# Kernel tuning notes

Hardware: AMD Instinct MI355X
Metric: run time of the kernel (lower is better)

Reference implementation:

```python
import jax, jax.numpy as jnp
import numpy as np

B, S, D = 4, 2048, 1024

def setup_inputs() -> dict:
    key = jax.random.key(0)
    ks = jax.random.split(key, 9)
    sc = 1.0 / np.sqrt(D)
    return {
        "x": jax.random.normal(ks[0], (B, S, D), dtype=jnp.float32),
        "Wq": jax.random.normal(ks[1], (D, D), dtype=jnp.float32) * sc,
        "bq": jnp.zeros((D,), dtype=jnp.float32),
        "Wk": jax.random.normal(ks[2], (D, D), dtype=jnp.float32) * sc,
        "bk": jnp.zeros((D,), dtype=jnp.float32),
        "Wv": jax.random.normal(ks[3], (D, D), dtype=jnp.float32) * sc,
        "bv": jnp.zeros((D,), dtype=jnp.float32),
        "Wo": jax.random.normal(ks[4], (D, D), dtype=jnp.float32) * sc,
        "bo": jnp.zeros((D,), dtype=jnp.float32),
    }

def _gaussian_mask(seq_len, dtype):
    # exp(-0.5*((pos - S/2)/(S/4))^2), shape [1,1,S] -> broadcasts over KEY axis
    pos = jnp.arange(seq_len, dtype=dtype)
    center = seq_len / 2
    sigma = seq_len / 4
    m = jnp.exp(-0.5 * ((pos - center) / sigma) ** 2)
    return m[None, None, :]

def reference(x, Wq, bq, Wk, bk, Wv, bv, Wo, bo):
    d = x.shape[-1]
    Q = x @ Wq.T + bq            # [B,S,D]
    K = x @ Wk.T + bk
    V = x @ Wv.T + bv
    scores = jnp.einsum('bqd,bkd->bqk', Q, K) / jnp.sqrt(jnp.asarray(d, x.dtype))
    scores = scores * _gaussian_mask(x.shape[1], x.dtype)
    attn = jax.nn.softmax(scores, axis=-1)
    out = jnp.einsum('bqk,bkd->bqd', attn, V)
    return out @ Wo.T + bo
```

## Files before the change

### kernel.cpp

```cpp
#include <hip/hip_runtime.h>
#include <math.h>

#define SEQ 2048
#define DIM 1024

typedef __attribute__((ext_vector_type(8))) _Float16 half8;
typedef __attribute__((ext_vector_type(4))) float f32x4;

__device__ __forceinline__ unsigned short f2h(float f) {
    union { _Float16 h; unsigned short u; } c; c.h = (_Float16)f;
    return c.u;
}
__device__ __forceinline__ float gmask(int k) {
    float t = ((float)k - 1024.0f) * (1.0f / 512.0f);
    return expf(-0.5f * t * t);
}
__device__ __forceinline__ void glds16(const unsigned short* gp, unsigned short* lp) {
    __builtin_amdgcn_global_load_lds((const __attribute__((address_space(1))) void*)gp,
                                     (__attribute__((address_space(3))) void*)lp, 16, 0, 0);
}

__device__ __forceinline__ void stage64(const unsigned short* __restrict__ g, int ldK,
                                        unsigned short* lds, int wave, int lane) {
    int row = wave * 32 + (lane >> 3);
    int seg = (lane & 7) ^ (lane >> 3);
    const unsigned short* gp = g + (long)row * ldK + seg * 8;
    unsigned short* lp = lds + wave * 2048;
    glds16(gp, lp);
    glds16(gp + 8 * (long)ldK, lp + 512);
    glds16(gp + 16 * (long)ldK, lp + 1024);
    glds16(gp + 24 * (long)ldK, lp + 1536);
}

enum { EPI_QKV = 0, EPI_EXP = 1, EPI_PV = 2, EPI_OUT = 3 };

template <int EPI>
__global__ __launch_bounds__(256, 4) void mfma_gemm(
    const unsigned short* __restrict__ A, const unsigned short* __restrict__ Bm,
    const float* __restrict__ bias,
    float* __restrict__ Cf, unsigned short* __restrict__ Ch,
    int M, int N, int K, float scale, long sA, long sB, long sC)
{
    __shared__ unsigned short As[128 * 64];
    __shared__ unsigned short Bs[128 * 64];

    const int bz = blockIdx.z;
    const int tid = threadIdx.x;
    const int wave = tid >> 6;
    const int lane = tid & 63;
    const int wm = (wave & 1) * 64;
    const int wn = (wave >> 1) * 64;
    const long m0 = (long)blockIdx.y * 128;
    const long n0 = (long)blockIdx.x * 128;
    const int lm = lane & 15;
    const int lk = lane >> 4;

    const unsigned short* pA = A + bz * sA + m0 * K;
    const unsigned short* pB = Bm + bz * sB + n0 * K;

    f32x4 acc[4][4];
#pragma unroll
    for (int i = 0; i < 4; ++i)
#pragma unroll
        for (int j = 0; j < 4; ++j) {
            acc[i][j].x = 0.f; acc[i][j].y = 0.f; acc[i][j].z = 0.f; acc[i][j].w = 0.f;
        }

    int aoff[4][2], boff[4][2];
#pragma unroll
    for (int i = 0; i < 4; ++i)
#pragma unroll
        for (int t = 0; t < 2; ++t) {
            int ar = wm + i * 16 + lm;
            aoff[i][t] = ar * 64 + (((4 * t + lk) ^ (ar & 7)) << 3);
            int br = wn + i * 16 + lm;
            boff[i][t] = br * 64 + (((4 * t + lk) ^ (br & 7)) << 3);
        }

    const int pr = (wave & 1) * 64 + lane;
    const int ph = wave >> 1;
    float psum = 0.f;

    for (int k0 = 0; k0 < K; k0 += 64) {
        stage64(pA + k0, K, As, wave, lane);
        stage64(pB + k0, K, Bs, wave, lane);
        __syncthreads();

        if (EPI == EPI_PV) {
            const unsigned short* rowp = As + pr * 64;
#pragma unroll
            for (int i2 = 0; i2 < 4; ++i2) {
                half8 h = *(const half8*)(rowp + (((2 * i2 + ph) ^ (pr & 7)) << 3));
#pragma unroll
                for (int e = 0; e < 8; ++e) psum += (float)h[e];
            }
        }

#pragma unroll
        for (int t = 0; t < 2; ++t) {
            half8 a[4], b[4];
#pragma unroll
            for (int i = 0; i < 4; ++i) a[i] = *(const half8*)(As + aoff[i][t]);
#pragma unroll
            for (int j = 0; j < 4; ++j) b[j] = *(const half8*)(Bs + boff[j][t]);
#pragma unroll
            for (int i = 0; i < 4; ++i)
#pragma unroll
                for (int j = 0; j < 4; ++j)
                    acc[i][j] = __builtin_amdgcn_mfma_f32_16x16x32_f16(a[i], b[j], acc[i][j], 0, 0, 0);
        }
        __syncthreads();
    }

    float* rsf = (float*)As;
    if (EPI == EPI_PV) {
        rsf[ph * 128 + pr] = psum;
        __syncthreads();
    }

    const long MD = 8388608;
    float* cF = (EPI == EPI_OUT) ? Cf + bz * sC : (float*)nullptr;
    unsigned short* cH = (EPI != EPI_OUT) ? Ch + bz * sC : (unsigned short*)nullptr;

#pragma unroll
    for (int i = 0; i < 4; ++i) {
        long mrow = m0 + wm + i * 16 + lk * 4;
        int lr = wm + i * 16 + lk * 4;
        float inv4[4];
        if (EPI == EPI_PV) {
#pragma unroll
            for (int r = 0; r < 4; ++r)
                inv4[r] = 1.0f / (rsf[lr + r] + rsf[128 + lr + r]);
        }
#pragma unroll
        for (int j = 0; j < 4; ++j) {
            int n = (int)n0 + wn + j * 16 + lm;
            if (EPI == EPI_QKV) {
                int sel = n >> 10;
                int n1 = n & 1023;
                float bs = bias[n];
                if (sel < 2) {
                    unsigned short* dst = cH + (long)sel * MD;
#pragma unroll
                    for (int r = 0; r < 4; ++r)
                        dst[(mrow + r) * (long)DIM + n1] = f2h(acc[i][j][r] + bs);
                } else {
                    long b = mrow >> 11, s = mrow & 2047;
                    long idx = 2 * MD + b * (long)DIM * SEQ + (long)n1 * SEQ + s;
                    unsigned long long pk =
                        (unsigned long long)f2h(acc[i][j].x + bs) |
                        ((unsigned long long)f2h(acc[i][j].y + bs) << 16) |
                        ((unsigned long long)f2h(acc[i][j].z + bs) << 32) |
                        ((unsigned long long)f2h(acc[i][j].w + bs) << 48);
                    *(unsigned long long*)(cH + idx) = pk;
                }
            } else if (EPI == EPI_EXP) {
                float mult = scale * gmask(n);
#pragma unroll
                for (int r = 0; r < 4; ++r)
                    cH[(mrow + r) * (long)N + n] = f2h(expf(acc[i][j][r] * mult));
            } else if (EPI == EPI_PV) {
#pragma unroll
                for (int r = 0; r < 4; ++r)
                    cH[(mrow + r) * (long)N + n] = f2h(acc[i][j][r] * inv4[r]);
            } else {
                float bs = bias[n];
#pragma unroll
                for (int r = 0; r < 4; ++r)
                    cF[(mrow + r) * (long)N + n] = acc[i][j][r] + bs;
            }
        }
    }
}

__global__ __launch_bounds__(256) void prep(
    const float* __restrict__ x,
    const float* __restrict__ Wq, const float* __restrict__ Wk,
    const float* __restrict__ Wv, const float* __restrict__ Wo,
    const float* __restrict__ b0, const float* __restrict__ b1, const float* __restrict__ b2,
    unsigned short* __restrict__ xh, unsigned short* __restrict__ Wp, float* __restrict__ bqkv)
{
    long gid = (long)blockIdx.x * 256 + threadIdx.x;
    if (gid < 3072) {
        int sel = (int)(gid >> 10);
        const float* s = sel == 0 ? b0 : sel == 1 ? b1 : b2;
        bqkv[gid] = s[gid & 1023];
    }
    const long NX = 8388608 / 4;
    const long NW = 1048576 / 4;
    const long total = NX + 4 * NW;
    for (long i = gid; i < total; i += (long)gridDim.x * 256) {
        const float* src; unsigned short* dst; long off;
        if (i < NX) { src = x; dst = xh; off = i; }
        else {
            long wi = i - NX;
            int sel = (int)(wi >> 18);
            src = sel == 0 ? Wq : sel == 1 ? Wk : sel == 2 ? Wv : Wo;
            dst = Wp + ((long)sel << 20);
            off = wi & (NW - 1);
        }
        float4 v = ((const float4*)src)[off];
        unsigned long long p = (unsigned long long)f2h(v.x) | ((unsigned long long)f2h(v.y) << 16) |
                               ((unsigned long long)f2h(v.z) << 32) | ((unsigned long long)f2h(v.w) << 48);
        ((unsigned long long*)dst)[off] = p;
    }
}

extern "C" void kernel_launch(void* const* d_in, const int* in_sizes, int n_in,
                              void* d_out, int out_size, void* d_ws, size_t ws_size,
                              hipStream_t stream)
{
    const float* x  = (const float*)d_in[0];
    const float* Wq = (const float*)d_in[1];
    const float* bq = (const float*)d_in[2];
    const float* Wk = (const float*)d_in[3];
    const float* bk = (const float*)d_in[4];
    const float* Wv = (const float*)d_in[5];
    const float* bv = (const float*)d_in[6];
    const float* Wo = (const float*)d_in[7];
    const float* bo = (const float*)d_in[8];
    float* out = (float*)d_out;

    const long MD = 4L * SEQ * DIM;
    const long WW = (long)DIM * DIM;
    const long SD = (long)SEQ * DIM, SS = (long)SEQ * SEQ;

    unsigned short* xh   = (unsigned short*)d_ws;
    unsigned short* Wp   = xh + MD;
    unsigned short* Woh  = Wp + 3 * WW;
    float* bqkv          = (float*)(Wp + 4 * WW);
    unsigned short* Qh   = (unsigned short*)(bqkv + 4096);
    unsigned short* VT   = Qh + 2 * MD;
    unsigned short* expS = Qh + 3 * MD;
    unsigned short* O1   = xh;

    dim3 blk(256);
    prep<<<4096, blk, 0, stream>>>(x, Wq, Wk, Wv, Wo, bq, bk, bv, xh, Wp, bqkv);

    mfma_gemm<EPI_QKV><<<dim3(3 * DIM / 128, (4 * SEQ) / 128, 1), blk, 0, stream>>>(
        xh, Wp, bqkv, nullptr, Qh, 4 * SEQ, 3 * DIM, DIM, 1.0f, 0, 0, 0);
    mfma_gemm<EPI_EXP><<<dim3(SEQ / 128, SEQ / 128, 4), blk, 0, stream>>>(
        Qh, Qh + MD, nullptr, nullptr, expS, SEQ, SEQ, DIM, 0.03125f, SD, SD, SS);
    mfma_gemm<EPI_PV><<<dim3(DIM / 128, SEQ / 128, 4), blk, 0, stream>>>(
        expS, VT, nullptr, nullptr, O1, SEQ, DIM, SEQ, 1.0f, SS, (long)DIM * SEQ, SD);
    mfma_gemm<EPI_OUT><<<dim3(DIM / 128, (4 * SEQ) / 128, 1), blk, 0, stream>>>(
        O1, Woh, bo, out, nullptr, 4 * SEQ, DIM, DIM, 1.0f, 0, 0, 0);
}
```

Before: 270.6 us.

## Pipeline GEMM with triple-buffered LDS, 128x256 tiles, and row sums moved to exp epilogue

Rewrites the shared MFMA GEMM to use 512-thread blocks computing 128x256 tiles. A three-stage LDS ring buffer with async global-to-LDS loads interleaves staging with MFMA phases, using explicit barriers, waitcnt and setprio to overlap memory and compute. The softmax row-sum is now computed in the exp epilogue via shuffles and atomics into a zeroed buffer, replacing the per-tile LDS reduction in the PV kernel. This adds more barriers per iteration and atomic traffic, and raises LDS usage, which may limit occupancy.

```diff
diff --git a/kernel.cpp b/kernel.cpp
--- a/kernel.cpp
+++ b/kernel.cpp
@@ -11,6 +11,10 @@
     union { _Float16 h; unsigned short u; } c; c.h = (_Float16)f;
     return c.u;
 }
+__device__ __forceinline__ float h2f(unsigned short u) {
+    union { unsigned short u2; _Float16 h; } c; c.u2 = u;
+    return (float)c.h;
+}
 __device__ __forceinline__ float gmask(int k) {
     float t = ((float)k - 1024.0f) * (1.0f / 512.0f);
     return expf(-0.5f * t * t);
@@ -20,38 +24,40 @@
                                      (__attribute__((address_space(3))) void*)lp, 16, 0, 0);
 }
 
-__device__ __forceinline__ void stage64(const unsigned short* __restrict__ g, int ldK,
-                                        unsigned short* lds, int wave, int lane) {
-    int row = wave * 32 + (lane >> 3);
+__device__ __forceinline__ void stage_unit(const unsigned short* __restrict__ g, int ldK,
+                                           unsigned short* lds, int wave, int lane) {
+    int row = wave * 16 + (lane >> 3);
     int seg = (lane & 7) ^ (lane >> 3);
     const unsigned short* gp = g + (long)row * ldK + seg * 8;
-    unsigned short* lp = lds + wave * 2048;
+    unsigned short* lp = lds + wave * 1024;
     glds16(gp, lp);
     glds16(gp + 8 * (long)ldK, lp + 512);
-    glds16(gp + 16 * (long)ldK, lp + 1024);
-    glds16(gp + 24 * (long)ldK, lp + 1536);
 }
 
 enum { EPI_QKV = 0, EPI_EXP = 1, EPI_PV = 2, EPI_OUT = 3 };
 
+#define BAR() __builtin_amdgcn_s_barrier()
+#define LGKM0() asm volatile("s_waitcnt lgkmcnt(0)" ::: "memory")
+#define VMC(N) asm volatile("s_waitcnt vmcnt(" #N ")" ::: "memory")
+
 template <int EPI>
-__global__ __launch_bounds__(256, 4) void mfma_gemm(
+__global__ __launch_bounds__(512, 2) void mfma_gemm(
     const unsigned short* __restrict__ A, const unsigned short* __restrict__ Bm,
-    const float* __restrict__ bias,
+    const float* __restrict__ aux,
     float* __restrict__ Cf, unsigned short* __restrict__ Ch,
+    float* __restrict__ rsum,
     int M, int N, int K, float scale, long sA, long sB, long sC)
 {
-    __shared__ unsigned short As[128 * 64];
-    __shared__ unsigned short Bs[128 * 64];
+    __shared__ unsigned short sh[3 * 24576];
 
     const int bz = blockIdx.z;
     const int tid = threadIdx.x;
     const int wave = tid >> 6;
     const int lane = tid & 63;
-    const int wm = (wave & 1) * 64;
-    const int wn = (wave >> 1) * 64;
+    const int rb = (wave & 1) * 64;
+    const int cb = (wave >> 1) * 64;
     const long m0 = (long)blockIdx.y * 128;
-    const long n0 = (long)blockIdx.x * 128;
+    const long n0 = (long)blockIdx.x * 256;
     const int lm = lane & 15;
     const int lk = lane >> 4;
 
@@ -68,54 +74,103 @@
 
     int aoff[4][2], boff[4][2];
 #pragma unroll
-    for (int i = 0; i < 4; ++i)
+    for (int f = 0; f < 4; ++f)
 #pragma unroll
         for (int t = 0; t < 2; ++t) {
-            int ar = wm + i * 16 + lm;
-            aoff[i][t] = ar * 64 + (((4 * t + lk) ^ (ar & 7)) << 3);
-            int br = wn + i * 16 + lm;
-            boff[i][t] = br * 64 + (((4 * t + lk) ^ (br & 7)) << 3);
-        }
-
-    const int pr = (wave & 1) * 64 + lane;
-    const int ph = wave >> 1;
-    float psum = 0.f;
-
-    for (int k0 = 0; k0 < K; k0 += 64) {
-        stage64(pA + k0, K, As, wave, lane);
-        stage64(pB + k0, K, Bs, wave, lane);
-        __syncthreads();
-
-        if (EPI == EPI_PV) {
-            const unsigned short* rowp = As + pr * 64;
-#pragma unroll
-            for (int i2 = 0; i2 < 4; ++i2) {
-                half8 h = *(const half8*)(rowp + (((2 * i2 + ph) ^ (pr & 7)) << 3));
-#pragma unroll
-                for (int e = 0; e < 8; ++e) psum += (float)h[e];
-            }
-        }
-
-#pragma unroll
-        for (int t = 0; t < 2; ++t) {
-            half8 a[4], b[4];
-#pragma unroll
-            for (int i = 0; i < 4; ++i) a[i] = *(const half8*)(As + aoff[i][t]);
-#pragma unroll
-            for (int j = 0; j < 4; ++j) b[j] = *(const half8*)(Bs + boff[j][t]);
-#pragma unroll
-            for (int i = 0; i < 4; ++i)
-#pragma unroll
-                for (int j = 0; j < 4; ++j)
-                    acc[i][j] = __builtin_amdgcn_mfma_f32_16x16x32_f16(a[i], b[j], acc[i][j], 0, 0, 0);
-        }
-        __syncthreads();
-    }
-
-    float* rsf = (float*)As;
-    if (EPI == EPI_PV) {
-        rsf[ph * 128 + pr] = psum;
-        __syncthreads();
+            int ar = rb + f * 16 + lm;
+            aoff[f][t] = ar * 64 + (((4 * t + lk) ^ (ar & 7)) << 3);
+            int br = cb + f * 16 + lm;
+            boff[f][t] = br * 64 + (((4 * t + lk) ^ (br & 7)) << 3);
+        }
+
+    const int NT = K >> 6;
+
+    stage_unit(pA, K, sh, wave, lane);
+    stage_unit(pB, K, sh + 8192, wave, lane);
+    stage_unit(pB + 128 * (long)K, K, sh + 16384, wave, lane);
+    stage_unit(pA + 64, K, sh + 24576, wave, lane);
+    stage_unit(pB + 64, K, sh + 24576 + 8192, wave, lane);
+    stage_unit(pB + 128 * (long)K + 64, K, sh + 24576 + 16384, wave, lane);
+    VMC(6);
+    BAR();
+
+#pragma unroll 1
+    for (int t = 0; t < NT; ++t) {
+        unsigned short* As = sh + (t % 3) * 24576;
+        unsigned short* Bs = As + 8192;
+        const int t2 = t + 2;
+        const bool st = t2 < NT;
+        unsigned short* Sd = sh + (t2 % 3) * 24576;
+
+        half8 a[2][2], b[4][2];
+
+#pragma unroll
+        for (int kt = 0; kt < 2; ++kt) {
+            a[0][kt] = *(const half8*)(As + aoff[0][kt]);
+            a[1][kt] = *(const half8*)(As + aoff[1][kt]);
+            b[0][kt] = *(const half8*)(Bs + boff[0][kt]);
+            b[1][kt] = *(const half8*)(Bs + boff[1][kt]);
+        }
+        if (st) stage_unit(pA + t2 * 64, K, Sd, wave, lane);
+        BAR(); LGKM0();
+        __builtin_amdgcn_s_setprio(1);
+#pragma unroll
+        for (int mi = 0; mi < 2; ++mi)
+#pragma unroll
+            for (int nj = 0; nj < 2; ++nj)
+#pragma unroll
+                for (int kt = 0; kt < 2; ++kt)
+                    acc[mi][nj] = __builtin_amdgcn_mfma_f32_16x16x32_f16(a[mi][kt], b[nj][kt], acc[mi][nj], 0, 0, 0);
+        __builtin_amdgcn_s_setprio(0);
+        BAR();
+
+#pragma unroll
+        for (int kt = 0; kt < 2; ++kt) {
+            b[2][kt] = *(const half8*)(Bs + boff[2][kt]);
+            b[3][kt] = *(const half8*)(Bs + boff[3][kt]);
+        }
+        if (st) stage_unit(pB + t2 * 64, K, Sd + 8192, wave, lane);
+        BAR(); LGKM0();
+        __builtin_amdgcn_s_setprio(1);
+#pragma unroll
+        for (int mi = 0; mi < 2; ++mi)
+#pragma unroll
+            for (int nj = 2; nj < 4; ++nj)
+#pragma unroll
+                for (int kt = 0; kt < 2; ++kt)
+                    acc[mi][nj] = __builtin_amdgcn_mfma_f32_16x16x32_f16(a[mi][kt], b[nj][kt], acc[mi][nj], 0, 0, 0);
+        __builtin_amdgcn_s_setprio(0);
+        BAR();
+
+#pragma unroll
+        for (int kt = 0; kt < 2; ++kt) {
+            a[0][kt] = *(const half8*)(As + aoff[2][kt]);
+            a[1][kt] = *(const half8*)(As + aoff[3][kt]);
+        }
+        if (st) stage_unit(pB + 128 * (long)K + t2 * 64, K, Sd + 16384, wave, lane);
+        BAR(); LGKM0();
+        __builtin_amdgcn_s_setprio(1);
+#pragma unroll
+        for (int mi = 0; mi < 2; ++mi)
+#pragma unroll
+            for (int nj = 2; nj < 4; ++nj)
+#pragma unroll
+                for (int kt = 0; kt < 2; ++kt)
+                    acc[2 + mi][nj] = __builtin_amdgcn_mfma_f32_16x16x32_f16(a[mi][kt], b[nj][kt], acc[2 + mi][nj], 0, 0, 0);
+        __builtin_amdgcn_s_setprio(0);
+        BAR();
+
+        __builtin_amdgcn_s_setprio(1);
+#pragma unroll
+        for (int mi = 0; mi < 2; ++mi)
+#pragma unroll
+            for (int nj = 0; nj < 2; ++nj)
+#pragma unroll
+                for (int kt = 0; kt < 2; ++kt)
+                    acc[2 + mi][nj] = __builtin_amdgcn_mfma_f32_16x16x32_f16(a[mi][kt], b[nj][kt], acc[2 + mi][nj], 0, 0, 0);
+        __builtin_amdgcn_s_setprio(0);
+        if (t < NT - 2) { VMC(6); } else { VMC(0); }
+        BAR();
     }
 
     const long MD = 8388608;
@@ -123,51 +178,74 @@
     unsigned short* cH = (EPI != EPI_OUT) ? Ch + bz * sC : (unsigned short*)nullptr;
 
 #pragma unroll
-    for (int i = 0; i < 4; ++i) {
-        long mrow = m0 + wm + i * 16 + lk * 4;
-        int lr = wm + i * 16 + lk * 4;
-        float inv4[4];
-        if (EPI == EPI_PV) {
-#pragma unroll
-            for (int r = 0; r < 4; ++r)
-                inv4[r] = 1.0f / (rsf[lr + r] + rsf[128 + lr + r]);
-        }
-#pragma unroll
-        for (int j = 0; j < 4; ++j) {
-            int n = (int)n0 + wn + j * 16 + lm;
-            if (EPI == EPI_QKV) {
+    for (int mf = 0; mf < 4; ++mf) {
+        long mrow = m0 + rb + mf * 16 + lk * 4;
+        if (EPI == EPI_QKV) {
+#pragma unroll
+            for (int nf = 0; nf < 4; ++nf) {
+                int n = (int)n0 + cb + nf * 16 + lm;
                 int sel = n >> 10;
                 int n1 = n & 1023;
-                float bs = bias[n];
+                float bs = aux[n];
                 if (sel < 2) {
                     unsigned short* dst = cH + (long)sel * MD;
 #pragma unroll
                     for (int r = 0; r < 4; ++r)
-                        dst[(mrow + r) * (long)DIM + n1] = f2h(acc[i][j][r] + bs);
+                        dst[(mrow + r) * (long)DIM + n1] = f2h(acc[mf][nf][r] + bs);
                 } else {
-                    long b = mrow >> 11, s = mrow & 2047;
-                    long idx = 2 * MD + b * (long)DIM * SEQ + (long)n1 * SEQ + s;
+                    long bb = mrow >> 11, s = mrow & 2047;
+                    long idx = 2 * MD + bb * (long)DIM * SEQ + (long)n1 * SEQ + s;
                     unsigned long long pk =
-                        (unsigned long long)f2h(acc[i][j].x + bs) |
-                        ((unsigned long long)f2h(acc[i][j].y + bs) << 16) |
-                        ((unsigned long long)f2h(acc[i][j].z + bs) << 32) |
-                        ((unsigned long long)f2h(acc[i][j].w + bs) << 48);
+                        (unsigned long long)f2h(acc[mf][nf].x + bs) |
+                        ((unsigned long long)f2h(acc[mf][nf].y + bs) << 16) |
+                        ((unsigned long long)f2h(acc[mf][nf].z + bs) << 32) |
+                        ((unsigned long long)f2h(acc[mf][nf].w + bs) << 48);
                     *(unsigned long long*)(cH + idx) = pk;
                 }
-            } else if (EPI == EPI_EXP) {
+            }
+        } else if (EPI == EPI_EXP) {
+            float rsv[4] = {0.f, 0.f, 0.f, 0.f};
+#pragma unroll
+            for (int nf = 0; nf < 4; ++nf) {
+                int n = (int)n0 + cb + nf * 16 + lm;
                 float mult = scale * gmask(n);
 #pragma unroll
+                for (int r = 0; r < 4; ++r) {
+                    float e = expf(acc[mf][nf][r] * mult);
+                    unsigned short h = f2h(e);
+                    cH[(mrow + r) * (long)N + n] = h;
+                    rsv[r] += h2f(h);
+                }
+            }
+#pragma unroll
+            for (int r = 0; r < 4; ++r) {
+#pragma unroll
+                for (int msk = 1; msk < 16; msk <<= 1)
+                    rsv[r] += __shfl_xor(rsv[r], msk, 64);
+            }
+            if (lm == 0) {
+#pragma unroll
                 for (int r = 0; r < 4; ++r)
-                    cH[(mrow + r) * (long)N + n] = f2h(expf(acc[i][j][r] * mult));
-            } else if (EPI == EPI_PV) {
+                    atomicAdd(rsum + (long)bz * SEQ + mrow + r, rsv[r]);
+            }
+        } else if (EPI == EPI_PV) {
+#pragma unroll
+            for (int r = 0; r < 4; ++r) {
+                float inv = 1.0f / rsum[(long)bz * SEQ + mrow + r];
+#pragma unroll
+                for (int nf = 0; nf < 4; ++nf) {
+                    int n = (int)n0 + cb + nf * 16 + lm;
+                    cH[(mrow + r) * (long)N + n] = f2h(acc[mf][nf][r] * inv);
+                }
+            }
+        } else {
+#pragma unroll
+            for (int nf = 0; nf < 4; ++nf) {
+                int n = (int)n0 + cb + nf * 16 + lm;
+                float bs = aux[n];
 #pragma unroll
                 for (int r = 0; r < 4; ++r)
-                    cH[(mrow + r) * (long)N + n] = f2h(acc[i][j][r] * inv4[r]);
-            } else {
-                float bs = bias[n];
-#pragma unroll
-                for (int r = 0; r < 4; ++r)
-                    cF[(mrow + r) * (long)N + n] = acc[i][j][r] + bs;
+                    cF[(mrow + r) * (long)N + n] = acc[mf][nf][r] + bs;
             }
         }
     }
@@ -178,7 +256,8 @@
     const float* __restrict__ Wq, const float* __restrict__ Wk,
     const float* __restrict__ Wv, const float* __restrict__ Wo,
     const float* __restrict__ b0, const float* __restrict__ b1, const float* __restrict__ b2,
-    unsigned short* __restrict__ xh, unsigned short* __restrict__ Wp, float* __restrict__ bqkv)
+    unsigned short* __restrict__ xh, unsigned short* __restrict__ Wp,
+    float* __restrict__ bqkv, float* __restrict__ rsum)
 {
     long gid = (long)blockIdx.x * 256 + threadIdx.x;
     if (gid < 3072) {
@@ -186,6 +265,7 @@
         const float* s = sel == 0 ? b0 : sel == 1 ? b1 : b2;
         bqkv[gid] = s[gid & 1023];
     }
+    if (gid < 4 * SEQ) rsum[gid] = 0.f;
     const long NX = 8388608 / 4;
     const long NW = 1048576 / 4;
     const long total = NX + 4 * NW;
@@ -232,17 +312,18 @@
     unsigned short* Qh   = (unsigned short*)(bqkv + 4096);
     unsigned short* VT   = Qh + 2 * MD;
     unsigned short* expS = Qh + 3 * MD;
+    float* rsum          = (float*)(expS + 4 * SS);
     unsigned short* O1   = xh;
 
-    dim3 blk(256);
-    prep<<<4096, blk, 0, stream>>>(x, Wq, Wk, Wv, Wo, bq, bk, bv, xh, Wp, bqkv);
-
-    mfma_gemm<EPI_QKV><<<dim3(3 * DIM / 128, (4 * SEQ) / 128, 1), blk, 0, stream>>>(
-        xh, Wp, bqkv, nullptr, Qh, 4 * SEQ, 3 * DIM, DIM, 1.0f, 0, 0, 0);
-    mfma_gemm<EPI_EXP><<<dim3(SEQ / 128, SEQ / 128, 4), blk, 0, stream>>>(
-        Qh, Qh + MD, nullptr, nullptr, expS, SEQ, SEQ, DIM, 0.03125f, SD, SD, SS);
-    mfma_gemm<EPI_PV><<<dim3(DIM / 128, SEQ / 128, 4), blk, 0, stream>>>(
-        expS, VT, nullptr, nullptr, O1, SEQ, DIM, SEQ, 1.0f, SS, (long)DIM * SEQ, SD);
-    mfma_gemm<EPI_OUT><<<dim3(DIM / 128, (4 * SEQ) / 128, 1), blk, 0, stream>>>(
-        O1, Woh, bo, out, nullptr, 4 * SEQ, DIM, DIM, 1.0f, 0, 0, 0);
-}
+    dim3 blk(512);
+    prep<<<4096, dim3(256), 0, stream>>>(x, Wq, Wk, Wv, Wo, bq, bk, bv, xh, Wp, bqkv, rsum);
+
+    mfma_gemm<EPI_QKV><<<dim3(3 * DIM / 256, (4 * SEQ) / 128, 1), blk, 0, stream>>>(
+        xh, Wp, bqkv, nullptr, Qh, nullptr, 4 * SEQ, 3 * DIM, DIM, 1.0f, 0, 0, 0);
+    mfma_gemm<EPI_EXP><<<dim3(SEQ / 256, SEQ / 128, 4), blk, 0, stream>>>(
+        Qh, Qh + MD, nullptr, nullptr, expS, rsum, SEQ, SEQ, DIM, 0.03125f, SD, SD, SS);
+    mfma_gemm<EPI_PV><<<dim3(DIM / 256, SEQ / 128, 4), blk, 0, stream>>>(
+        expS, VT, nullptr, nullptr, O1, rsum, SEQ, DIM, SEQ, 1.0f, SS, (long)DIM * SEQ, SD);
+    mfma_gemm<EPI_OUT><<<dim3(DIM / 256, (4 * SEQ) / 128, 1), blk, 0, stream>>>(
+        O1, Woh, bo, out, nullptr, nullptr, 4 * SEQ, DIM, DIM, 1.0f, 0, 0, 0);
+}
```

New measurement: 293.4 us. +8.4%, slower.
